# Kernel optimization log

Measured on AMD Instinct MI355X. Metric: run time of the kernel, lower is better.

The kernel has to match this reference:

```python
import jax, jax.numpy as jnp
import numpy as np

B = 128   # graphs in batch
N = 512   # nodes per graph (max nodes, static)
D = 128   # in_features_node
C = 64    # num_clusters
DEG = 16  # average degree -> E = B*N*DEG
EPS = 1e-15


def setup_inputs() -> dict:
    key = jax.random.key(0)
    k1, k2, k3, k4, k5, k6 = jax.random.split(key, 6)
    total = B * N
    x = jax.random.normal(k1, (total, D), dtype=jnp.float32)
    # edges are intra-graph: pick graph g, local endpoints u, v
    E = total * DEG
    g = jax.random.randint(k2, (E,), 0, B, dtype=jnp.int32)
    u = jax.random.randint(k3, (E,), 0, N, dtype=jnp.int32)
    v = jax.random.randint(k4, (E,), 0, N, dtype=jnp.int32)
    edge_index = jnp.stack([g * N + u, g * N + v]).astype(jnp.int32)
    batch = jnp.repeat(jnp.arange(B, dtype=jnp.int32), N)  # sorted graph ids
    scale = 1.0 / np.sqrt(D)
    W_rel = jax.random.normal(k5, (C, D), dtype=jnp.float32) * scale   # lin_rel (no bias)
    W_root = jax.random.normal(k6, (C, D), dtype=jnp.float32) * scale  # lin_root
    b_root = jnp.zeros((C,), dtype=jnp.float32)
    return {"x": x, "edge_index": edge_index, "batch": batch,
            "W_rel": W_rel, "W_root": W_root, "b_root": b_root}


def reference(x, edge_index, batch, W_rel, W_root, b_root):
    total = x.shape[0]
    # --- to_dense_batch ---
    counts = jax.ops.segment_sum(jnp.ones(total, jnp.int32), batch, num_segments=B)
    ptr = jnp.concatenate([jnp.zeros(1, jnp.int32), jnp.cumsum(counts).astype(jnp.int32)])
    pos = jnp.arange(total, dtype=jnp.int32) - ptr[batch]  # intra-graph index
    dense_x = jnp.zeros((B, N, D), x.dtype).at[batch, pos].set(x)
    mask = jnp.zeros((B, N), bool).at[batch, pos].set(True)
    # --- to_dense_adj (scatter-add ones; duplicate edges accumulate, as in PyG) ---
    src, dst = edge_index[0], edge_index[1]
    b_e = batch[src]
    adj = jnp.zeros((B, N, N), x.dtype).at[b_e, pos[src], pos[dst]].add(1.0)
    # --- DenseSAGEConv(D -> C), normalize=False, mask not passed ---
    agg = jnp.matmul(adj, dense_x)                            # [B,N,D]
    agg = agg / jnp.clip(jnp.sum(adj, axis=-1, keepdims=True), 1.0)
    s_logits = agg @ W_rel.T + dense_x @ W_root.T + b_root    # [B,N,C]
    # --- dense_diff_pool ---
    s = jax.nn.softmax(s_logits, axis=-1)
    m = mask[..., None].astype(x.dtype)
    xm = dense_x * m
    sm = s * m
    out_x = jnp.einsum('bnc,bnd->bcd', sm, xm)                # S^T X  [B,C,D]
    sta = jnp.einsum('bnc,bnm->bcm', sm, adj)                 # S^T A  [B,C,N]
    out_adj = jnp.einsum('bcm,bmk->bck', sta, sm)             # S^T A S [B,C,C]
    link = adj - jnp.matmul(sm, jnp.swapaxes(sm, 1, 2))       # A - S S^T
    link_loss = jnp.linalg.norm(link.reshape(-1)) / float(B * N * N)
    ent_loss = jnp.mean(jnp.sum(-sm * jnp.log(sm + EPS), axis=-1))
    x_out = out_x.reshape(B * C, D)
    new_batch = jnp.repeat(jnp.arange(B, dtype=jnp.int32), C)
    # dense_to_sparse(out_adj) has data-dependent shape; out_adj is returned dense
    # (softmax-pooled adjacency is generically fully dense) -- see notes.
    return (x_out, out_adj, new_batch, link_loss, ent_loss)
```

## Files before the change

### kernel.cpp

```cpp
#include <hip/hip_runtime.h>
#include <math.h>

#define B_ 128
#define N_ 512
#define D_ 128
#define C_ 64
#define TOT 65536
#define E_ 1048576
#define GCAP 12288
#define YSTR 68

#define L0 (B_*C_*D_)
#define L1 (B_*C_*C_)
#define L2 (B_*C_)

static const size_t OFF_SCAL   = 0;
static const size_t OFF_FILLG  = 256;
static const size_t OFF_ROWS   = 1024;
static const size_t OFF_BINNED = 1024 + 262656;
static const size_t OFF_CSR16  = OFF_BINNED + (size_t)B_*GCAP*4;
static const size_t OFF_S      = OFF_CSR16 + (size_t)B_*GCAP*2;
static const size_t OFF_Y      = OFF_S + (size_t)TOT*C_*4;
static const size_t OFF_Z      = OFF_Y + (size_t)TOT*64*4;


__global__ __launch_bounds__(512) void k_gb(const int* __restrict__ ei,
    unsigned* __restrict__ fillg, unsigned* __restrict__ binned,
    const float* __restrict__ x, const float* __restrict__ W_rel,
    const float* __restrict__ W_root, float* __restrict__ Yb, float* __restrict__ Zb){
  __shared__ __align__(16) float smem[2*32*132];
  int t = threadIdx.x;
  int bid = (int)blockIdx.x;
  if (bid < 256){
    char* sb8 = (char*)smem;
    unsigned* cnt  = (unsigned*)(sb8);
    unsigned* sb   = (unsigned*)(sb8 + 512);
    unsigned* fl   = (unsigned*)(sb8 + 1024);
    unsigned* gd   = (unsigned*)(sb8 + 1536);
    unsigned* wsum = (unsigned*)(sb8 + 2048);
    unsigned* stage= (unsigned*)(sb8 + 2064);
    int e0 = bid * 4096;
    if (t < 128) cnt[t] = 0;
    __syncthreads();
    for (int i = t; i < 4096; i += 512)
      atomicAdd(&cnt[((unsigned)ei[e0+i]) >> 9], 1u);
    __syncthreads();
    unsigned v = 0, orig = 0;
    if (t < 128){
      v = cnt[t]; orig = v;
      #pragma unroll
      for (int d = 1; d < 64; d <<= 1){
        unsigned o = __shfl_up(v, d);
        if ((t & 63) >= d) v += o;
      }
      if ((t & 63) == 63) wsum[t >> 6] = v;
    }
    __syncthreads();
    if (t < 128){
      unsigned ex = ((t >= 64) ? wsum[0] : 0u) + v - orig;
      sb[t] = ex; fl[t] = ex;
      gd[t] = (unsigned)(t*GCAP) + atomicAdd(&fillg[t], cnt[t]);
    }
    __syncthreads();
    for (int i = t; i < 4096; i += 512){
      unsigned s0 = (unsigned)ei[e0+i], d0 = (unsigned)ei[E_+e0+i];
      unsigned g = s0 >> 9;
      unsigned pay = (g << 18) | ((s0 & 511u) << 9) | (d0 & 511u);
      unsigned p = atomicAdd(&fl[g], 1u);
      stage[p] = pay;
    }
    __syncthreads();
    for (int i = t; i < 4096; i += 512){
      unsigned e = stage[i];
      unsigned g = e >> 18;
      binned[gd[g] + (i - sb[g])] = e;
    }
  } else {
    float (*aT)[132] = (float(*)[132])smem;
    float (*bT)[132] = (float(*)[132])((char*)smem + 16896);
    int m0 = (bid - 256) * 128;
    int tm = t & 31, tn = t >> 5;
    float acc[4][8] = {};
    for (int kt = 0; kt < 4; ++kt){
      __syncthreads();
      #pragma unroll
      for (int it = 0; it < 2; ++it){
        int idx = it*512 + t;
        int k4 = idx & 7, row = idx >> 3;
        float4 v = *(const float4*)&x[(size_t)(m0+row)*128 + kt*32 + k4*4];
        aT[k4*4+0][row] = v.x; aT[k4*4+1][row] = v.y;
        aT[k4*4+2][row] = v.z; aT[k4*4+3][row] = v.w;
      }
      #pragma unroll
      for (int it = 0; it < 2; ++it){
        int idx = it*512 + t;
        int k4 = idx & 7, n = idx >> 3;
        const float* Wsrc = (n < 64) ? &W_rel[(size_t)n*128] : &W_root[(size_t)(n-64)*128];
        float4 v = *(const float4*)&Wsrc[kt*32 + k4*4];
        bT[k4*4+0][n] = v.x; bT[k4*4+1][n] = v.y;
        bT[k4*4+2][n] = v.z; bT[k4*4+3][n] = v.w;
      }
      __syncthreads();
      #pragma unroll 4
      for (int k = 0; k < 32; ++k){
        float4 a0 = *(const float4*)&aT[k][tm*4];
        float4 b0 = *(const float4*)&bT[k][tn*8];
        float4 b1 = *(const float4*)&bT[k][tn*8+4];
        float av[4] = {a0.x,a0.y,a0.z,a0.w};
        float bv[8] = {b0.x,b0.y,b0.z,b0.w,b1.x,b1.y,b1.z,b1.w};
        #pragma unroll
        for (int i=0;i<4;i++){
          #pragma unroll
          for (int j=0;j<8;j++) acc[i][j] += av[i]*bv[j];
        }
      }
    }
    float* base = (tn < 8) ? Yb : Zb;
    int col = (tn & 7) * 8;
    #pragma unroll
    for (int i = 0; i < 4; ++i){
      float* dst = &base[(size_t)(m0 + tm*4 + i)*64 + col];
      *(float4*)dst     = make_float4(acc[i][0],acc[i][1],acc[i][2],acc[i][3]);
      *(float4*)(dst+4) = make_float4(acc[i][4],acc[i][5],acc[i][6],acc[i][7]);
    }
  }
}

__global__ __launch_bounds__(256) void k_build(const unsigned* __restrict__ binned,
    const unsigned* __restrict__ fillg, unsigned* __restrict__ rows,
    unsigned short* __restrict__ csr16){
  __shared__ unsigned cnt[512], fill2[512];
  __shared__ unsigned wsum[4];
  __shared__ unsigned short svals[GCAP];
  int t = threadIdx.x, g = blockIdx.x;
  int base = g * GCAP;
  int m = (int)fillg[g];
  cnt[t] = 0; cnt[t+256] = 0;
  __syncthreads();
  for (int i = t; i < m; i += 256)
    atomicAdd(&cnt[(binned[base+i] >> 9) & 511u], 1u);
  __syncthreads();
  unsigned a = cnt[2*t], b = cnt[2*t+1];
  unsigned v = a + b, orig = v;
  #pragma unroll
  for (int d = 1; d < 64; d <<= 1){
    unsigned o = __shfl_up(v, d);
    if ((t & 63) >= d) v += o;
  }
  if ((t & 63) == 63) wsum[t >> 6] = v;
  __syncthreads();
  unsigned woff = 0;
  for (int w = 0; w < (t >> 6); ++w) woff += wsum[w];
  unsigned ex = woff + v - orig;
  fill2[2*t] = ex; fill2[2*t+1] = ex + a;
  rows[g*513 + 2*t]   = (unsigned)base + ex;
  rows[g*513 + 2*t+1] = (unsigned)base + ex + a;
  if (t == 0) rows[g*513 + 512] = (unsigned)(base + m);
  __syncthreads();
  for (int i = t; i < m; i += 256){
    unsigned e = binned[base+i];
    unsigned p = atomicAdd(&fill2[(e >> 9) & 511u], 1u);
    svals[p] = (unsigned short)(e & 511u);
  }
  __syncthreads();
  for (int i = t; i < m; i += 256) csr16[base+i] = svals[i];
}

__global__ __launch_bounds__(1024, 4) void k_finish(const float* __restrict__ Yb,
    const float* __restrict__ Zb, const unsigned* __restrict__ rows,
    const unsigned short* __restrict__ csr16, const float* __restrict__ b_root,
    float* __restrict__ s, float* __restrict__ scal){
  __shared__ __align__(16) float Ylds[512*YSTR];
  __shared__ unsigned short csrl[10240];
  __shared__ unsigned rowl[513];
  __shared__ float r1[16], r2[16];
  int t = threadIdx.x;
  int lane = t & 63, wv = t >> 6;
  int c = lane & 31, hb = lane & 32;
  int bid = (int)blockIdx.x;
  int wg = (bid & 7)*32 + (bid >> 3);
  int g = wg >> 1, half = wg & 1;
  int base = g * GCAP;
  int m = (int)rows[g*513 + 512] - base;
  const float4* Ysrc = (const float4*)(Yb + ((size_t)g << 9)*64);
  for (int q = t; q < 8192; q += 1024){
    int r = q >> 4, cc = (q & 15) << 2;
    *(float4*)&Ylds[r*YSTR + cc] = Ysrc[q];
  }
  const unsigned* csrc = (const unsigned*)(csr16 + (size_t)base);
  int mw = (m + 1) >> 1; if (mw > 5120) mw = 5120;
  for (int q = t; q < mw; q += 1024) ((unsigned*)csrl)[q] = csrc[q];
  if (t < 513) rowl[t] = rows[g*513 + t] - (unsigned)base;
  __syncthreads();

  float2 br = *(const float2*)&b_root[2*c];
  float ent_local = 0.f, asq_local = 0.f;
  for (int it = 0; it < 8; ++it){
    int l = half*256 + it*32 + wv*2 + (hb >> 5);
    unsigned r0 = rowl[l];
    int deg = (int)(rowl[l+1] - r0);
    float2 acc = make_float2(0.f, 0.f);
    int cnt = 0;
    if (deg <= 32){
      unsigned val = (c < deg) ? (unsigned)csrl[r0 + c] : (0x10000u + (unsigned)lane);
      for (int j0 = 0; j0 < deg; j0 += 8){
        float2 yv[8]; unsigned vj[8];
        #pragma unroll
        for (int jj = 0; jj < 8; ++jj){
          vj[jj] = __shfl(val, hb + j0 + jj);
          yv[jj] = *(const float2*)&Ylds[(vj[jj] & 511u)*YSTR + 2*c];
        }
        #pragma unroll
        for (int jj = 0; jj < 8; ++jj){
          if (j0 + jj < deg){
            acc.x += yv[jj].x; acc.y += yv[jj].y;
            cnt += (val == vj[jj]);
          }
        }
      }
    } else {
      for (int j = 0; j < deg; ++j){
        float2 y = *(const float2*)&Ylds[(unsigned)csrl[r0+j]*YSTR + 2*c];
        acc.x += y.x; acc.y += y.y;
      }
      int dd = deg*deg;
      for (int idx = c; idx < dd; idx += 32){
        int i2 = idx / deg, j2 = idx - i2*deg;
        cnt += (csrl[r0+i2] == csrl[r0+j2]) ? 1 : 0;
      }
    }
    int u = (g << 9) + l;
    float invdeg = 1.f / (float)(deg > 0 ? deg : 1);
    float2 zb = *(const float2*)&Zb[(size_t)u*64 + 2*c];
    float lx = acc.x*invdeg + zb.x + br.x;
    float ly = acc.y*invdeg + zb.y + br.y;
    float ex = __expf(lx), ey = __expf(ly);
    float ssum = ex + ey;
    #pragma unroll
    for (int d = 1; d < 32; d <<= 1) ssum += __shfl_xor(ssum, d);
    float inv = 1.f / ssum;
    float sx = ex*inv, sy = ey*inv;
    *(float2*)&s[(size_t)u*64 + 2*c] = make_float2(sx, sy);
    ent_local += -(sx*__logf(sx + 1e-15f) + sy*__logf(sy + 1e-15f));
    asq_local += (float)cnt;
  }
  float v1 = ent_local, v2 = asq_local;
  #pragma unroll
  for (int d=1; d<64; d<<=1){ v1 += __shfl_xor(v1, d); v2 += __shfl_xor(v2, d); }
  if (lane==0){ r1[wv]=v1; r2[wv]=v2; }
  __syncthreads();
  if (t==0){
    float a1 = 0.f, a2 = 0.f;
    #pragma unroll
    for (int w = 0; w < 16; ++w){ a1 += r1[w]; a2 += r2[w]; }
    atomicAdd(&scal[3], a1);
    atomicAdd(&scal[0], a2);
  }
}

__global__ __launch_bounds__(1024, 4) void k_gatherR(const float* __restrict__ s,
    const unsigned* __restrict__ rows, const unsigned short* __restrict__ csr16,
    float* __restrict__ R){
  __shared__ __align__(16) float Slds[512*YSTR];
  __shared__ unsigned short csrl[10240];
  __shared__ unsigned rowl[513];
  int t = threadIdx.x;
  int lane = t & 63, wv = t >> 6;
  int c = lane & 31, hb = lane & 32;
  int bid = (int)blockIdx.x;
  int wg = (bid & 7)*32 + (bid >> 3);
  int g = wg >> 1, half = wg & 1;
  int base = g * GCAP;
  int m = (int)rows[g*513 + 512] - base;
  const float4* Ssrc = (const float4*)(s + ((size_t)g << 9)*64);
  for (int q = t; q < 8192; q += 1024){
    int r = q >> 4, cc = (q & 15) << 2;
    *(float4*)&Slds[r*YSTR + cc] = Ssrc[q];
  }
  const unsigned* csrc = (const unsigned*)(csr16 + (size_t)base);
  int mw = (m + 1) >> 1; if (mw > 5120) mw = 5120;
  for (int q = t; q < mw; q += 1024) ((unsigned*)csrl)[q] = csrc[q];
  if (t < 513) rowl[t] = rows[g*513 + t] - (unsigned)base;
  __syncthreads();

  for (int it = 0; it < 8; ++it){
    int l = half*256 + it*32 + wv*2 + (hb >> 5);
    unsigned r0 = rowl[l];
    int deg = (int)(rowl[l+1] - r0);
    float2 tv = make_float2(0.f, 0.f);
    if (deg <= 32){
      unsigned val = (c < deg) ? (unsigned)csrl[r0 + c] : 0u;
      for (int j0 = 0; j0 < deg; j0 += 8){
        float2 yv[8];
        #pragma unroll
        for (int jj = 0; jj < 8; ++jj){
          unsigned vj = __shfl(val, hb + j0 + jj);
          yv[jj] = *(const float2*)&Slds[vj*YSTR + 2*c];
        }
        #pragma unroll
        for (int jj = 0; jj < 8; ++jj){
          if (j0 + jj < deg){ tv.x += yv[jj].x; tv.y += yv[jj].y; }
        }
      }
    } else {
      for (int j = 0; j < deg; ++j){
        float2 y = *(const float2*)&Slds[(unsigned)csrl[r0+j]*YSTR + 2*c];
        tv.x += y.x; tv.y += y.y;
      }
    }
    int u = (g << 9) + l;
    *(float2*)&R[(size_t)u*64 + 2*c] = tv;
  }
}

__global__ __launch_bounds__(512) void k_pool3(const float* __restrict__ s,
    const float* __restrict__ x, const float* __restrict__ R,
    float* __restrict__ outx, float* __restrict__ outadj, float* __restrict__ scal){
  __shared__ __align__(16) float sbuf[2][32][64];
  __shared__ __align__(16) float dbuf[2][32][128];
  int t = threadIdx.x;
  int tm = t >> 8, tt = t & 255;
  int tc = tt & 15, td = tt >> 4;
  int c0 = tc*4, d0 = td*8;
  int bid = (int)blockIdx.x;
  int wg = (bid & 7)*32 + (bid >> 3);
  int g = wg >> 1, p = wg & 1;
  int nbase = g * N_;
  float acc[4][8];
  #pragma unroll
  for (int i=0;i<4;i++){
    #pragma unroll
    for (int j=0;j<8;j++) acc[i][j]=0.f;
  }
  for (int ch8 = 0; ch8 < 8; ++ch8){
    __syncthreads();
    int n0 = nbase + (ch8*2 + tm)*32;
    const float4* sp = (const float4*)&s[(size_t)n0*64];
    ((float4*)sbuf[tm])[tt]       = sp[tt];
    ((float4*)sbuf[tm])[tt+256]   = sp[tt+256];
    if (p == 0){
      const float4* xp = (const float4*)&x[(size_t)n0*128];
      #pragma unroll
      for (int k = 0; k < 4; ++k)
        ((float4*)dbuf[tm])[tt + k*256] = xp[tt + k*256];
    } else {
      const float4* spp = (const float4*)&s[(size_t)n0*64];
      const float4* rpp = (const float4*)&R[(size_t)n0*64];
      #pragma unroll
      for (int k = 0; k < 4; ++k){
        int q = tt + k*256;
        int n = q >> 5, sub = q & 31;
        ((float4*)dbuf[tm])[q] = (sub < 16) ? spp[(n<<4) + sub] : rpp[(n<<4) + sub - 16];
      }
    }
    __syncthreads();
    #pragma unroll 4
    for (int n = 0; n < 32; ++n){
      float4 s4 = *(const float4*)&sbuf[tm][n][c0];
      const float4* dr = (const float4*)&dbuf[tm][n][d0];
      float4 dA = dr[0], dB = dr[1];
      float dv[8] = {dA.x,dA.y,dA.z,dA.w,dB.x,dB.y,dB.z,dB.w};
      float sv[4] = {s4.x,s4.y,s4.z,s4.w};
      #pragma unroll
      for (int i=0;i<4;i++){
        #pragma unroll
        for (int j=0;j<8;j++) acc[i][j] += sv[i]*dv[j];
      }
    }
  }
  __syncthreads();
  float* red = (float*)dbuf;
  if (tm == 1){
    #pragma unroll
    for (int i=0;i<4;i++)
      #pragma unroll
      for (int j=0;j<8;j++) red[tt*32 + i*8 + j] = acc[i][j];
  }
  __syncthreads();
  if (tm == 0){
    #pragma unroll
    for (int i=0;i<4;i++)
      #pragma unroll
      for (int j=0;j<8;j++) acc[i][j] += red[tt*32 + i*8 + j];
    if (p == 0){
      #pragma unroll
      for (int i=0;i<4;i++){
        float* dst = &outx[((size_t)g*C_ + c0+i)*D_ + d0];
        *(float4*)dst     = make_float4(acc[i][0],acc[i][1],acc[i][2],acc[i][3]);
        *(float4*)(dst+4) = make_float4(acc[i][4],acc[i][5],acc[i][6],acc[i][7]);
      }
    } else {
      float ss = 0.f, tr = 0.f;
      if (td < 8){
        #pragma unroll
        for (int i=0;i<4;i++)
          #pragma unroll
          for (int j=0;j<8;j++) ss += acc[i][j]*acc[i][j];
      } else {
        int a0 = (td-8)*8;
        #pragma unroll
        for (int i=0;i<4;i++){
          float* dst = &outadj[((size_t)g*C_ + c0+i)*C_ + a0];
          *(float4*)dst     = make_float4(acc[i][0],acc[i][1],acc[i][2],acc[i][3]);
          *(float4*)(dst+4) = make_float4(acc[i][4],acc[i][5],acc[i][6],acc[i][7]);
          int dd = (c0+i) - a0;
          if (dd >= 0 && dd < 8) tr += acc[i][dd];
        }
      }
      #pragma unroll
      for (int d=1; d<64; d<<=1){
        ss += __shfl_xor(ss, d);
        tr += __shfl_xor(tr, d);
      }
      if ((tt & 63) == 0){
        atomicAdd(&scal[2], ss);
        atomicAdd(&scal[1], tr);
      }
    }
  }
}

__global__ void k_final(float* __restrict__ out, const float* __restrict__ scal){
  int i = blockIdx.x*256 + threadIdx.x;
  if (i < L2) out[L0+L1+i] = (float)(i >> 6);
  if (i == 0){
    float asq = scal[0], adot = scal[1], gsq = scal[2], ent = scal[3];
    float lsq = asq - 2.f*adot + gsq;
    out[L0+L1+L2]   = sqrtf(fmaxf(lsq, 0.f)) / 33554432.f;
    out[L0+L1+L2+1] = ent / (float)TOT;
  }
}

extern "C" void kernel_launch(void* const* d_in, const int* in_sizes, int n_in,
                              void* d_out, int out_size, void* d_ws, size_t ws_size,
                              hipStream_t stream){
  const float* x      = (const float*)d_in[0];
  const int*   ei     = (const int*)d_in[1];
  const float* W_rel  = (const float*)d_in[3];
  const float* W_root = (const float*)d_in[4];
  const float* b_root = (const float*)d_in[5];
  float* out = (float*)d_out;
  char*  ws  = (char*)d_ws;

  float*    scal    = (float*)(ws + OFF_SCAL);
  unsigned* fillg   = (unsigned*)(ws + OFF_FILLG);
  unsigned* rows    = (unsigned*)(ws + OFF_ROWS);
  unsigned* binned  = (unsigned*)(ws + OFF_BINNED);
  unsigned short* csr16 = (unsigned short*)(ws + OFF_CSR16);
  float*    s       = (float*)(ws + OFF_S);
  float*    Yb      = (float*)(ws + OFF_Y);
  float*    Zb      = (float*)(ws + OFF_Z);
  float*    R       = Yb;

  hipMemsetAsync(ws, 0, 1024, stream);

  k_gb     <<<768,    512, 0, stream>>>(ei, fillg, binned, x, W_rel, W_root, Yb, Zb);
  k_build  <<<B_,     256, 0, stream>>>(binned, fillg, rows, csr16);
  k_finish <<<256,   1024, 0, stream>>>(Yb, Zb, rows, csr16, b_root, s, scal);
  k_gatherR<<<256,   1024, 0, stream>>>(s, rows, csr16, R);
  k_pool3  <<<B_*2,   512, 0, stream>>>(s, x, R, out, out + L0, scal);
  k_final  <<<32,     256, 0, stream>>>(out, scal);
}
```

Measured before the change: 159.5 us.

## Split pooling across node halves with a reduce kernel; shrink projection GEMM tiles

The pooling kernel now splits each graph's node range into two halves, so twice as many workgroups run. Each writes a partial S^T[X|S|R] tile to workspace, and a new reduce kernel sums the two halves, writes the outputs and computes the trace and squared-norm scalars. The fused edge-binning/projection kernel also moves to 256-thread blocks with 64-row GEMM tiles, launching more blocks for the projection. This aims to fill the GPU better, at the cost of an extra kernel launch and a round trip of partial results through global memory.

```diff
diff --git a/kernel.cpp b/kernel.cpp
--- a/kernel.cpp
+++ b/kernel.cpp
@@ -24,11 +24,11 @@
 static const size_t OFF_Z      = OFF_Y + (size_t)TOT*64*4;
 
 
-__global__ __launch_bounds__(512) void k_gb(const int* __restrict__ ei,
+__global__ __launch_bounds__(256) void k_gb(const int* __restrict__ ei,
     unsigned* __restrict__ fillg, unsigned* __restrict__ binned,
     const float* __restrict__ x, const float* __restrict__ W_rel,
     const float* __restrict__ W_root, float* __restrict__ Yb, float* __restrict__ Zb){
-  __shared__ __align__(16) float smem[2*32*132];
+  __shared__ __align__(16) float smem[6400];
   int t = threadIdx.x;
   int bid = (int)blockIdx.x;
   if (bid < 256){
@@ -42,7 +42,7 @@
     int e0 = bid * 4096;
     if (t < 128) cnt[t] = 0;
     __syncthreads();
-    for (int i = t; i < 4096; i += 512)
+    for (int i = t; i < 4096; i += 256)
       atomicAdd(&cnt[((unsigned)ei[e0+i]) >> 9], 1u);
     __syncthreads();
     unsigned v = 0, orig = 0;
@@ -62,7 +62,7 @@
       gd[t] = (unsigned)(t*GCAP) + atomicAdd(&fillg[t], cnt[t]);
     }
     __syncthreads();
-    for (int i = t; i < 4096; i += 512){
+    for (int i = t; i < 4096; i += 256){
       unsigned s0 = (unsigned)ei[e0+i], d0 = (unsigned)ei[E_+e0+i];
       unsigned g = s0 >> 9;
       unsigned pay = (g << 18) | ((s0 & 511u) << 9) | (d0 & 511u);
@@ -70,30 +70,30 @@
       stage[p] = pay;
     }
     __syncthreads();
-    for (int i = t; i < 4096; i += 512){
+    for (int i = t; i < 4096; i += 256){
       unsigned e = stage[i];
       unsigned g = e >> 18;
       binned[gd[g] + (i - sb[g])] = e;
     }
   } else {
-    float (*aT)[132] = (float(*)[132])smem;
-    float (*bT)[132] = (float(*)[132])((char*)smem + 16896);
-    int m0 = (bid - 256) * 128;
-    int tm = t & 31, tn = t >> 5;
+    float (*aT)[68]  = (float(*)[68])smem;
+    float (*bT)[132] = (float(*)[132])((char*)smem + 8704);
+    int m0 = (bid - 256) * 64;
+    int tm = t & 15, tn = t >> 4;
     float acc[4][8] = {};
     for (int kt = 0; kt < 4; ++kt){
       __syncthreads();
       #pragma unroll
       for (int it = 0; it < 2; ++it){
-        int idx = it*512 + t;
+        int idx = it*256 + t;
         int k4 = idx & 7, row = idx >> 3;
         float4 v = *(const float4*)&x[(size_t)(m0+row)*128 + kt*32 + k4*4];
         aT[k4*4+0][row] = v.x; aT[k4*4+1][row] = v.y;
         aT[k4*4+2][row] = v.z; aT[k4*4+3][row] = v.w;
       }
       #pragma unroll
-      for (int it = 0; it < 2; ++it){
-        int idx = it*512 + t;
+      for (int it = 0; it < 4; ++it){
+        int idx = it*256 + t;
         int k4 = idx & 7, n = idx >> 3;
         const float* Wsrc = (n < 64) ? &W_rel[(size_t)n*128] : &W_root[(size_t)(n-64)*128];
         float4 v = *(const float4*)&Wsrc[kt*32 + k4*4];
@@ -313,9 +313,8 @@
   }
 }
 
-__global__ __launch_bounds__(512) void k_pool3(const float* __restrict__ s,
-    const float* __restrict__ x, const float* __restrict__ R,
-    float* __restrict__ outx, float* __restrict__ outadj, float* __restrict__ scal){
+__global__ __launch_bounds__(512) void k_pool4(const float* __restrict__ s,
+    const float* __restrict__ x, const float* __restrict__ R, float* __restrict__ P){
   __shared__ __align__(16) float sbuf[2][32][64];
   __shared__ __align__(16) float dbuf[2][32][128];
   int t = threadIdx.x;
@@ -323,22 +322,22 @@
   int tc = tt & 15, td = tt >> 4;
   int c0 = tc*4, d0 = td*8;
   int bid = (int)blockIdx.x;
-  int wg = (bid & 7)*32 + (bid >> 3);
-  int g = wg >> 1, p = wg & 1;
-  int nbase = g * N_;
+  int wg = (bid & 7)*64 + (bid >> 3);
+  int g = wg >> 2, part = (wg >> 1) & 1, nh = wg & 1;
+  int nbase = g*N_ + nh*256;
   float acc[4][8];
   #pragma unroll
   for (int i=0;i<4;i++){
     #pragma unroll
     for (int j=0;j<8;j++) acc[i][j]=0.f;
   }
-  for (int ch8 = 0; ch8 < 8; ++ch8){
-    __syncthreads();
-    int n0 = nbase + (ch8*2 + tm)*32;
+  for (int ch4 = 0; ch4 < 4; ++ch4){
+    __syncthreads();
+    int n0 = nbase + (ch4*2 + tm)*32;
     const float4* sp = (const float4*)&s[(size_t)n0*64];
     ((float4*)sbuf[tm])[tt]       = sp[tt];
     ((float4*)sbuf[tm])[tt+256]   = sp[tt+256];
-    if (p == 0){
+    if (part == 0){
       const float4* xp = (const float4*)&x[(size_t)n0*128];
       #pragma unroll
       for (int k = 0; k < 4; ++k)
@@ -378,44 +377,54 @@
   }
   __syncthreads();
   if (tm == 0){
-    #pragma unroll
-    for (int i=0;i<4;i++)
+    float* dst = &P[(size_t)wg*8192];
+    #pragma unroll
+    for (int i=0;i<4;i++){
       #pragma unroll
       for (int j=0;j<8;j++) acc[i][j] += red[tt*32 + i*8 + j];
-    if (p == 0){
-      #pragma unroll
-      for (int i=0;i<4;i++){
-        float* dst = &outx[((size_t)g*C_ + c0+i)*D_ + d0];
-        *(float4*)dst     = make_float4(acc[i][0],acc[i][1],acc[i][2],acc[i][3]);
-        *(float4*)(dst+4) = make_float4(acc[i][4],acc[i][5],acc[i][6],acc[i][7]);
-      }
+      float* dr = &dst[(size_t)(c0+i)*128 + d0];
+      *(float4*)dr     = make_float4(acc[i][0],acc[i][1],acc[i][2],acc[i][3]);
+      *(float4*)(dr+4) = make_float4(acc[i][4],acc[i][5],acc[i][6],acc[i][7]);
+    }
+  }
+}
+
+__global__ __launch_bounds__(256) void k_reduce(const float* __restrict__ P,
+    float* __restrict__ outx, float* __restrict__ outadj, float* __restrict__ scal){
+  int bid = (int)blockIdx.x;
+  int g = bid >> 1, part = bid & 1;
+  const float* p0 = &P[(size_t)(g*4 + part*2)*8192];
+  const float* p1 = p0 + 8192;
+  int t = threadIdx.x;
+  float gsq = 0.f, tr = 0.f;
+  for (int it = 0; it < 8; ++it){
+    int e = it*1024 + t*4;
+    float4 a = *(const float4*)&p0[e];
+    float4 b = *(const float4*)&p1[e];
+    float4 v = make_float4(a.x+b.x, a.y+b.y, a.z+b.z, a.w+b.w);
+    if (part == 0){
+      *(float4*)&outx[(size_t)g*8192 + e] = v;
     } else {
-      float ss = 0.f, tr = 0.f;
-      if (td < 8){
-        #pragma unroll
-        for (int i=0;i<4;i++)
-          #pragma unroll
-          for (int j=0;j<8;j++) ss += acc[i][j]*acc[i][j];
+      int c = e >> 7, d = e & 127;
+      if (d < 64){
+        gsq += v.x*v.x + v.y*v.y + v.z*v.z + v.w*v.w;
       } else {
-        int a0 = (td-8)*8;
-        #pragma unroll
-        for (int i=0;i<4;i++){
-          float* dst = &outadj[((size_t)g*C_ + c0+i)*C_ + a0];
-          *(float4*)dst     = make_float4(acc[i][0],acc[i][1],acc[i][2],acc[i][3]);
-          *(float4*)(dst+4) = make_float4(acc[i][4],acc[i][5],acc[i][6],acc[i][7]);
-          int dd = (c0+i) - a0;
-          if (dd >= 0 && dd < 8) tr += acc[i][dd];
-        }
-      }
-      #pragma unroll
-      for (int d=1; d<64; d<<=1){
-        ss += __shfl_xor(ss, d);
-        tr += __shfl_xor(tr, d);
-      }
-      if ((tt & 63) == 0){
-        atomicAdd(&scal[2], ss);
-        atomicAdd(&scal[1], tr);
-      }
+        int dd = d - 64;
+        *(float4*)&outadj[(size_t)g*4096 + c*64 + dd] = v;
+        int k = c - dd;
+        if (k >= 0 && k < 4) tr += (k==0) ? v.x : (k==1) ? v.y : (k==2) ? v.z : v.w;
+      }
+    }
+  }
+  if (part == 1){
+    #pragma unroll
+    for (int d=1; d<64; d<<=1){
+      gsq += __shfl_xor(gsq, d);
+      tr  += __shfl_xor(tr, d);
+    }
+    if ((t & 63) == 0){
+      atomicAdd(&scal[2], gsq);
+      atomicAdd(&scal[1], tr);
     }
   }
 }
@@ -451,13 +460,15 @@
   float*    Yb      = (float*)(ws + OFF_Y);
   float*    Zb      = (float*)(ws + OFF_Z);
   float*    R       = Yb;
+  float*    P       = Zb;
 
   hipMemsetAsync(ws, 0, 1024, stream);
 
-  k_gb     <<<768,    512, 0, stream>>>(ei, fillg, binned, x, W_rel, W_root, Yb, Zb);
+  k_gb     <<<1280,   256, 0, stream>>>(ei, fillg, binned, x, W_rel, W_root, Yb, Zb);
   k_build  <<<B_,     256, 0, stream>>>(binned, fillg, rows, csr16);
   k_finish <<<256,   1024, 0, stream>>>(Yb, Zb, rows, csr16, b_root, s, scal);
   k_gatherR<<<256,   1024, 0, stream>>>(s, rows, csr16, R);
-  k_pool3  <<<B_*2,   512, 0, stream>>>(s, x, R, out, out + L0, scal);
+  k_pool4  <<<512,    512, 0, stream>>>(s, x, R, P);
+  k_reduce <<<256,    256, 0, stream>>>(P, out, out + L0, scal);
   k_final  <<<32,     256, 0, stream>>>(out, scal);
 }
```

Result: slower. 164.3 us (+3.0%).

## Use bf16 MFMA for pooling GEMMs with transposed LDS staging

Applied to the files above, without the earlier changes.

Replaces the scalar FP32 outer-product pooling kernel with a bf16 MFMA version. The s, x and R tiles are converted to bf16 and written to LDS transposed, 256 nodes per chunk, and each wave computes 16x64 output tiles with mfma_f32_16x16x32_bf16. The goal is to cut the FMA cost of the S^T X and S^T[S|R] products. The price is bf16 rounding in the outputs and loss terms, plus scalar strided global loads and 2-byte transposed LDS writes that may cause bank conflicts.

```diff
diff --git a/kernel.cpp b/kernel.cpp
--- a/kernel.cpp
+++ b/kernel.cpp
@@ -9,6 +9,7 @@
 #define E_ 1048576
 #define GCAP 12288
 #define YSTR 68
+#define KP 264
 
 #define L0 (B_*C_*D_)
 #define L1 (B_*C_*C_)
@@ -23,6 +24,14 @@
 static const size_t OFF_Y      = OFF_S + (size_t)TOT*C_*4;
 static const size_t OFF_Z      = OFF_Y + (size_t)TOT*64*4;
 
+
+typedef __attribute__((ext_vector_type(8))) short bf16x8;
+typedef __attribute__((ext_vector_type(4))) float f32x4;
+
+__device__ inline unsigned short f2bf(float f){
+  unsigned u = __float_as_uint(f);
+  return (unsigned short)((u + 0x7FFFu + ((u >> 16) & 1u)) >> 16);
+}
 
 __global__ __launch_bounds__(512) void k_gb(const int* __restrict__ ei,
     unsigned* __restrict__ fillg, unsigned* __restrict__ binned,
@@ -313,109 +322,88 @@
   }
 }
 
-__global__ __launch_bounds__(512) void k_pool3(const float* __restrict__ s,
+__global__ __launch_bounds__(512) void k_poolM(const float* __restrict__ s,
     const float* __restrict__ x, const float* __restrict__ R,
     float* __restrict__ outx, float* __restrict__ outadj, float* __restrict__ scal){
-  __shared__ __align__(16) float sbuf[2][32][64];
-  __shared__ __align__(16) float dbuf[2][32][128];
+  __shared__ __align__(16) unsigned short Abuf[64*KP];
+  __shared__ __align__(16) unsigned short Bbuf[128*KP];
   int t = threadIdx.x;
-  int tm = t >> 8, tt = t & 255;
-  int tc = tt & 15, td = tt >> 4;
-  int c0 = tc*4, d0 = td*8;
   int bid = (int)blockIdx.x;
   int wg = (bid & 7)*32 + (bid >> 3);
   int g = wg >> 1, p = wg & 1;
-  int nbase = g * N_;
-  float acc[4][8];
-  #pragma unroll
-  for (int i=0;i<4;i++){
-    #pragma unroll
-    for (int j=0;j<8;j++) acc[i][j]=0.f;
-  }
-  for (int ch8 = 0; ch8 < 8; ++ch8){
-    __syncthreads();
-    int n0 = nbase + (ch8*2 + tm)*32;
-    const float4* sp = (const float4*)&s[(size_t)n0*64];
-    ((float4*)sbuf[tm])[tt]       = sp[tt];
-    ((float4*)sbuf[tm])[tt+256]   = sp[tt+256];
+  int gbase = g * N_;
+  int w = t >> 6, l = t & 63;
+  int lr = l & 15, lg = l >> 4;
+  int ct = w & 3, dh = w >> 2;
+  f32x4 acc0 = {0.f,0.f,0.f,0.f}, acc1 = acc0, acc2 = acc0, acc3 = acc0;
+  const unsigned short* Amat = (p == 0) ? Abuf : Bbuf;
+  for (int chunk = 0; chunk < 2; ++chunk){
+    __syncthreads();
+    int k0 = chunk*256;
     if (p == 0){
-      const float4* xp = (const float4*)&x[(size_t)n0*128];
-      #pragma unroll
-      for (int k = 0; k < 4; ++k)
-        ((float4*)dbuf[tm])[tt + k*256] = xp[tt + k*256];
+      for (int q = t; q < 16384; q += 512){
+        int c = q & 63, n = q >> 6;
+        Abuf[c*KP + n] = f2bf(s[(size_t)(gbase+k0+n)*64 + c]);
+      }
+      for (int q = t; q < 32768; q += 512){
+        int d = q & 127, n = q >> 7;
+        Bbuf[d*KP + n] = f2bf(x[(size_t)(gbase+k0+n)*128 + d]);
+      }
     } else {
-      const float4* spp = (const float4*)&s[(size_t)n0*64];
-      const float4* rpp = (const float4*)&R[(size_t)n0*64];
-      #pragma unroll
-      for (int k = 0; k < 4; ++k){
-        int q = tt + k*256;
-        int n = q >> 5, sub = q & 31;
-        ((float4*)dbuf[tm])[q] = (sub < 16) ? spp[(n<<4) + sub] : rpp[(n<<4) + sub - 16];
-      }
-    }
-    __syncthreads();
-    #pragma unroll 4
-    for (int n = 0; n < 32; ++n){
-      float4 s4 = *(const float4*)&sbuf[tm][n][c0];
-      const float4* dr = (const float4*)&dbuf[tm][n][d0];
-      float4 dA = dr[0], dB = dr[1];
-      float dv[8] = {dA.x,dA.y,dA.z,dA.w,dB.x,dB.y,dB.z,dB.w};
-      float sv[4] = {s4.x,s4.y,s4.z,s4.w};
-      #pragma unroll
-      for (int i=0;i<4;i++){
-        #pragma unroll
-        for (int j=0;j<8;j++) acc[i][j] += sv[i]*dv[j];
-      }
-    }
-  }
-  __syncthreads();
-  float* red = (float*)dbuf;
-  if (tm == 1){
-    #pragma unroll
-    for (int i=0;i<4;i++)
-      #pragma unroll
-      for (int j=0;j<8;j++) red[tt*32 + i*8 + j] = acc[i][j];
-  }
-  __syncthreads();
-  if (tm == 0){
-    #pragma unroll
-    for (int i=0;i<4;i++)
-      #pragma unroll
-      for (int j=0;j<8;j++) acc[i][j] += red[tt*32 + i*8 + j];
-    if (p == 0){
-      #pragma unroll
-      for (int i=0;i<4;i++){
-        float* dst = &outx[((size_t)g*C_ + c0+i)*D_ + d0];
-        *(float4*)dst     = make_float4(acc[i][0],acc[i][1],acc[i][2],acc[i][3]);
-        *(float4*)(dst+4) = make_float4(acc[i][4],acc[i][5],acc[i][6],acc[i][7]);
-      }
+      for (int q = t; q < 16384; q += 512){
+        int c = q & 63, n = q >> 6;
+        size_t idx = (size_t)(gbase+k0+n)*64 + c;
+        Bbuf[c*KP + n]      = f2bf(s[idx]);
+        Bbuf[(64+c)*KP + n] = f2bf(R[idx]);
+      }
+    }
+    __syncthreads();
+    #pragma unroll
+    for (int ks = 0; ks < 8; ++ks){
+      bf16x8 a = *(const bf16x8*)&Amat[(ct*16 + lr)*KP + ks*32 + lg*8];
+      bf16x8 b0 = *(const bf16x8*)&Bbuf[(dh*64 +  0 + lr)*KP + ks*32 + lg*8];
+      bf16x8 b1 = *(const bf16x8*)&Bbuf[(dh*64 + 16 + lr)*KP + ks*32 + lg*8];
+      bf16x8 b2 = *(const bf16x8*)&Bbuf[(dh*64 + 32 + lr)*KP + ks*32 + lg*8];
+      bf16x8 b3 = *(const bf16x8*)&Bbuf[(dh*64 + 48 + lr)*KP + ks*32 + lg*8];
+      acc0 = __builtin_amdgcn_mfma_f32_16x16x32_bf16(a, b0, acc0, 0, 0, 0);
+      acc1 = __builtin_amdgcn_mfma_f32_16x16x32_bf16(a, b1, acc1, 0, 0, 0);
+      acc2 = __builtin_amdgcn_mfma_f32_16x16x32_bf16(a, b2, acc2, 0, 0, 0);
+      acc3 = __builtin_amdgcn_mfma_f32_16x16x32_bf16(a, b3, acc3, 0, 0, 0);
+    }
+  }
+  int crow0 = ct*16 + lg*4;
+  f32x4 av[4] = {acc0, acc1, acc2, acc3};
+  if (p == 0){
+    #pragma unroll
+    for (int dt = 0; dt < 4; ++dt)
+      #pragma unroll
+      for (int r = 0; r < 4; ++r)
+        outx[((size_t)(g*64 + crow0 + r))*128 + dh*64 + dt*16 + lr] = av[dt][r];
+  } else {
+    float ss = 0.f, tr = 0.f;
+    if (dh == 0){
+      #pragma unroll
+      for (int dt = 0; dt < 4; ++dt)
+        #pragma unroll
+        for (int r = 0; r < 4; ++r) ss += av[dt][r]*av[dt][r];
     } else {
-      float ss = 0.f, tr = 0.f;
-      if (td < 8){
-        #pragma unroll
-        for (int i=0;i<4;i++)
-          #pragma unroll
-          for (int j=0;j<8;j++) ss += acc[i][j]*acc[i][j];
-      } else {
-        int a0 = (td-8)*8;
-        #pragma unroll
-        for (int i=0;i<4;i++){
-          float* dst = &outadj[((size_t)g*C_ + c0+i)*C_ + a0];
-          *(float4*)dst     = make_float4(acc[i][0],acc[i][1],acc[i][2],acc[i][3]);
-          *(float4*)(dst+4) = make_float4(acc[i][4],acc[i][5],acc[i][6],acc[i][7]);
-          int dd = (c0+i) - a0;
-          if (dd >= 0 && dd < 8) tr += acc[i][dd];
-        }
-      }
-      #pragma unroll
-      for (int d=1; d<64; d<<=1){
-        ss += __shfl_xor(ss, d);
-        tr += __shfl_xor(tr, d);
-      }
-      if ((tt & 63) == 0){
-        atomicAdd(&scal[2], ss);
-        atomicAdd(&scal[1], tr);
-      }
+      #pragma unroll
+      for (int dt = 0; dt < 4; ++dt)
+        #pragma unroll
+        for (int r = 0; r < 4; ++r){
+          int cc = crow0 + r, dd = dt*16 + lr;
+          outadj[((size_t)(g*64 + cc))*64 + dd] = av[dt][r];
+          if (cc == dd) tr += av[dt][r];
+        }
+    }
+    #pragma unroll
+    for (int d = 1; d < 64; d <<= 1){
+      ss += __shfl_xor(ss, d);
+      tr += __shfl_xor(tr, d);
+    }
+    if (l == 0){
+      if (dh == 0) atomicAdd(&scal[2], ss);
+      else         atomicAdd(&scal[1], tr);
     }
   }
 }
@@ -458,6 +446,6 @@
   k_build  <<<B_,     256, 0, stream>>>(binned, fillg, rows, csr16);
   k_finish <<<256,   1024, 0, stream>>>(Yb, Zb, rows, csr16, b_root, s, scal);
   k_gatherR<<<256,   1024, 0, stream>>>(s, rows, csr16, R);
-  k_pool3  <<<B_*2,   512, 0, stream>>>(s, x, R, out, out + L0, scal);
+  k_poolM  <<<B_*2,   512, 0, stream>>>(s, x, R, out, out + L0, scal);
   k_final  <<<32,     256, 0, stream>>>(out, scal);
 }
```

Measured after the change: 142.2 us. 10.9% less time.
